# Performance work log

Measured on AMD Instinct MI355X. Metric: run time of the kernel, lower is better.

The kernel has to match this reference:

```python
import jax, jax.numpy as jnp
import numpy as np

B, S, D_IN = 2, 2048, 1024
H = 16
HD = 64  # head_dim = d_out // head_cnt


def setup_inputs() -> dict:
    key = jax.random.key(0)
    kx, kq, kk, kv = jax.random.split(key, 4)
    x = jax.random.normal(kx, (B, S, D_IN), dtype=jnp.float32)
    # Per-head Q/K/V projection weights, stacked: [H, d_in, head_dim].
    # Matches nn.Linear(d_in, head_out) per head (qkv_bias=False), scaled like
    # a typical init.
    sc = 1.0 / np.sqrt(D_IN)
    Wq = jax.random.normal(kq, (H, D_IN, HD), dtype=jnp.float32) * sc
    Wk = jax.random.normal(kk, (H, D_IN, HD), dtype=jnp.float32) * sc
    Wv = jax.random.normal(kv, (H, D_IN, HD), dtype=jnp.float32) * sc
    return {"x": x, "Wq": Wq, "Wk": Wk, "Wv": Wv}


def reference(x, Wq, Wk, Wv):
    # Batched multi-head causal attention equivalent to the per-head loop +
    # torch.cat(dim=-1): head h's output occupies slice [h*HD:(h+1)*HD].
    q = jnp.einsum("bsd,hde->bhse", x, Wq)  # [B,H,S,HD]
    k = jnp.einsum("bsd,hde->bhse", x, Wk)
    v = jnp.einsum("bsd,hde->bhse", x, Wv)
    scale = 1.0 / jnp.sqrt(jnp.asarray(HD, dtype=x.dtype))
    scores = jnp.einsum("bhse,bhte->bhst", q, k) * scale  # [B,H,S,S]
    seq = x.shape[1]
    causal = jnp.tril(jnp.ones((seq, seq), dtype=bool))
    scores = jnp.where(causal, scores, jnp.asarray(-jnp.inf, dtype=scores.dtype))
    attn = jax.nn.softmax(scores, axis=-1)  # dropout = 0.0 -> identity
    ctx = jnp.einsum("bhst,bhte->bhse", attn, v)  # [B,H,S,HD]
    # concat heads on last dim
    b, h, s, e = ctx.shape
    return ctx.transpose(0, 2, 1, 3).reshape(b, s, h * e)
```

## Files before the change

kernel.cpp:

```cpp
#include <hip/hip_runtime.h>


#define DI   1024
#define HD   64
#define NH   16
#define SEQ  2048
#define NB   2

typedef unsigned short u16;
typedef unsigned short us8 __attribute__((ext_vector_type(8)));
typedef unsigned short us4 __attribute__((ext_vector_type(4)));
typedef unsigned int   u32x2 __attribute__((ext_vector_type(2)));
typedef short bf8 __attribute__((ext_vector_type(8)));
typedef float f4 __attribute__((ext_vector_type(4)));
typedef float f16v __attribute__((ext_vector_type(16)));

#define MFMA16(a, b, c) __builtin_amdgcn_mfma_f32_16x16x32_bf16((a), (b), (c), 0, 0, 0)
#define MFMA32(a, b, c) __builtin_amdgcn_mfma_f32_32x32x16_bf16((a), (b), (c), 0, 0, 0)

#if __has_builtin(__builtin_amdgcn_exp2f)
#define EXP2(x) __builtin_amdgcn_exp2f(x)
#else
#define EXP2(x) exp2f(x)
#endif

#if __has_builtin(__builtin_amdgcn_perm)
#define PKHI(a, b) __builtin_amdgcn_perm((a), (b), 0x07060302u)
#else
__device__ __forceinline__ unsigned PKHI(unsigned a, unsigned b) {
  return (b >> 16) | (a & 0xffff0000u);
}
#endif

__device__ __forceinline__ u16 f2bf(float f) {
  unsigned u = __float_as_uint(f);
  u += 0x7fffu + ((u >> 16) & 1u);
  return (u16)(u >> 16);
}

__device__ __forceinline__ void async16(const u16* g, u16* l) {
  __builtin_amdgcn_global_load_lds((const __attribute__((address_space(1))) void*)g,
                                   (__attribute__((address_space(3))) void*)l,
                                   16, 0, 0);
}

__global__ __launch_bounds__(256) void prep_k(const float* __restrict__ x,
                                              const float* __restrict__ Wq,
                                              const float* __restrict__ Wk,
                                              const float* __restrict__ Wv,
                                              u16* __restrict__ xb,
                                              u16* __restrict__ Wt) {
  __shared__ __align__(16) u16 tile[64][72];
  const int bid = blockIdx.x;
  if (bid < 2048) {
    const int i = (bid * 256 + threadIdx.x) * 8;
    float4 v0 = *(const float4*)(x + i);
    float4 v1 = *(const float4*)(x + i + 4);
    us8 o;
    o[0] = f2bf(v0.x); o[1] = f2bf(v0.y); o[2] = f2bf(v0.z); o[3] = f2bf(v0.w);
    o[4] = f2bf(v1.x); o[5] = f2bf(v1.y); o[6] = f2bf(v1.z); o[7] = f2bf(v1.w);
    *(us8*)(xb + i) = o;
    return;
  }
  const int idx = bid - 2048;
  const int mh = idx >> 4;
  const int d0 = (idx & 15) * 64;
  const int mat = mh >> 4, h = mh & 15;
  const float* W = (mat == 0 ? Wq : (mat == 1 ? Wk : Wv)) + (size_t)h * DI * HD;
  const int t = threadIdx.x;
  {
    const int r = t >> 2, c = (t & 3) * 16;
    const float* src = W + (size_t)(d0 + r) * HD + c;
    #pragma unroll
    for (int j = 0; j < 4; j++) {
      float4 v = *(const float4*)(src + j * 4);
      tile[r][c + j * 4 + 0] = f2bf(v.x);
      tile[r][c + j * 4 + 1] = f2bf(v.y);
      tile[r][c + j * 4 + 2] = f2bf(v.z);
      tile[r][c + j * 4 + 3] = f2bf(v.w);
    }
  }
  __syncthreads();
  {
    const int e = t >> 2, c = (t & 3) * 16;
    __align__(16) u16 tmp[16];
    #pragma unroll
    for (int i = 0; i < 16; i++) tmp[i] = tile[c + i][e];
    u16* dst = Wt + ((size_t)mh * HD + e) * DI + d0 + c;
    *(us8*)dst       = *(us8*)&tmp[0];
    *(us8*)(dst + 8) = *(us8*)&tmp[8];
  }
}

__global__ __launch_bounds__(256, 2) void proj_k(const u16* __restrict__ x,
                                                 const u16* __restrict__ Wt,
                                                 u16* __restrict__ Qo,
                                                 u16* __restrict__ Ko,
                                                 u16* __restrict__ Vo) {
  __shared__ __align__(16) u16 smem[40960];
  u16* const xs = smem;
  u16* const ws = smem + 16384;
  const int m0 = blockIdx.x * 128, n0 = blockIdx.y * 192;
  const int tid = threadIdx.x, w = tid >> 6, lane = tid & 63;
  const int l15 = lane & 15, quad = lane >> 4, l7 = l15 & 7;
  const int lrow = lane >> 3, lch = lane & 7;
  const int wm = w >> 1, wn = w & 1;

  f4 acc[4][6];
  #pragma unroll
  for (int i = 0; i < 4; i++)
    #pragma unroll
    for (int j = 0; j < 6; j++) {
      f4 z = {0.f, 0.f, 0.f, 0.f};
      acc[i][j] = z;
    }

  const u16* xg = x  + (size_t)(m0 + lrow) * DI + ((lch ^ lrow) * 8);
  const u16* wg = Wt + (size_t)(n0 + lrow) * DI + ((lch ^ lrow) * 8);

  #pragma unroll
  for (int i = 0; i < 4; i++)
    async16(xg + (size_t)(i * 32 + w * 8) * DI, &xs[(i * 32 + w * 8) * 64]);
  #pragma unroll
  for (int c = 0; c < 6; c++)
    async16(wg + (size_t)(w * 48 + c * 8) * DI, &ws[(w * 48 + c * 8) * 64]);

  for (int it = 0; it < 16; it++) {
    const int cbx = (it & 1) * 8192, cbw = (it & 1) * 12288;
    __syncthreads();
    if (it + 1 < 16) {
      const int k1 = (it + 1) * 64;
      const int nbx = 8192 - cbx, nbw = 12288 - cbw;
      #pragma unroll
      for (int i = 0; i < 4; i++)
        async16(xg + (size_t)(i * 32 + w * 8) * DI + k1,
                &xs[nbx + (i * 32 + w * 8) * 64]);
      #pragma unroll
      for (int c = 0; c < 6; c++)
        async16(wg + (size_t)(w * 48 + c * 8) * DI + k1,
                &ws[nbw + (w * 48 + c * 8) * 64]);
    }
    #pragma unroll
    for (int ks = 0; ks < 64; ks += 32) {
      const int c0 = (ks >> 3) + quad;
      bf8 af[4], bfr[6];
      #pragma unroll
      for (int i = 0; i < 4; i++)
        af[i] = *(const bf8*)&xs[cbx + (wm * 64 + i * 16 + l15) * 64 + ((c0 ^ l7) * 8)];
      #pragma unroll
      for (int i = 0; i < 6; i++)
        bfr[i] = *(const bf8*)&ws[cbw + (wn * 96 + i * 16 + l15) * 64 + ((c0 ^ l7) * 8)];
      #pragma unroll
      for (int mi = 0; mi < 4; mi++)
        #pragma unroll
        for (int ni = 0; ni < 6; ni++)
          acc[mi][ni] = MFMA16(af[mi], bfr[ni], acc[mi][ni]);
    }
  }

  const float qscale = 0.125f * 1.44269504088896340736f;
  #pragma unroll
  for (int mi = 0; mi < 4; mi++) {
    const int mrow = m0 + wm * 64 + mi * 16 + quad * 4;
    const int b = mrow >> 11, sb = mrow & (SEQ - 1);
    #pragma unroll
    for (int ni = 0; ni < 6; ni++) {
      const int nf = n0 + wn * 96 + ni * 16;
      const int mat = nf >> 10;
      const int h = (nf >> 6) & 15;
      const int e = (nf & 63) + l15;
      if (mat == 2) {
        __align__(8) u16 pk[4];
        #pragma unroll
        for (int r = 0; r < 4; r++) pk[r] = f2bf(acc[mi][ni][r]);
        *(us4*)(Vo + (((size_t)b * NH + h) * HD + e) * SEQ + sb) = *(us4*)pk;
      } else {
        u16* O = mat ? Ko : Qo;
        const float sc = mat ? 1.0f : qscale;
        #pragma unroll
        for (int r = 0; r < 4; r++)
          O[(((size_t)b * NH + h) * SEQ + sb + r) * HD + e] = f2bf(acc[mi][ni][r] * sc);
      }
    }
  }
}

__global__ __launch_bounds__(256, 2) void attn_k(const u16* __restrict__ Qo,
                                                 const u16* __restrict__ Ko,
                                                 const u16* __restrict__ Vo,
                                                 float* __restrict__ out) {
  __shared__ __align__(16) u16 Ks[2 * 128 * 64];
  __shared__ __align__(16) u16 Vs[2 * 64 * 128];
  __shared__ float Ls[128];
  const int bh = blockIdx.x;
  const int y  = blockIdx.y;
  const int t  = (y < 8) ? y : 23 - y;
  const int b = bh >> 4, h = bh & 15;
  const int tid = threadIdx.x, w = tid >> 6, lane = tid & 63;
  const int l31 = lane & 31, hi = lane >> 5;
  const int k7 = l31 & 7, v15 = l31 & 15;
  const int nI = t + 1;

  const u16* Qb = Qo + (size_t)bh * SEQ * HD;
  const u16* Kb = Ko + (size_t)bh * SEQ * HD;
  const u16* Vb = Vo + (size_t)bh * HD * SEQ;

  const int kl = lane >> 3, kc = lane & 7;
  const int vl = lane >> 4, vc = lane & 15;
  const int mq = w * 32 + l31;

  bf8 bq[4];
  #pragma unroll
  for (int ks = 0; ks < 4; ks++)
    bq[ks] = *(const bf8*)(Qb + (size_t)(t * 128 + w * 32 + l31) * HD + ks * 16 + hi * 8);

  f16v o0, o1, zf;
  #pragma unroll
  for (int i = 0; i < 16; i++) { o0[i] = 0.f; o1[i] = 0.f; zf[i] = 0.f; }
  float lsum = 0.f;

  const u16* kg = Kb + (size_t)(w * 32 + kl) * HD + ((kc ^ kl) * 8);
  const u16* vg[4];
  u16* ldsK[4];
  u16* ldsV[4];
  #pragma unroll
  for (int i = 0; i < 4; i++) {
    const int vr = w * 16 + i * 4;
    const int f = (i * 4 + vl) & 15;
    vg[i] = Vb + (size_t)(vr + vl) * SEQ + ((vc ^ f) * 8);
    ldsK[i] = &Ks[(w * 32 + i * 8) * 64];
    ldsV[i] = &Vs[vr * 128];
  }

  #pragma unroll
  for (int i = 0; i < 4; i++) {
    async16(kg + i * 512, ldsK[i]);
    async16(vg[i], ldsV[i]);
  }
  kg += 128 * HD;
  #pragma unroll
  for (int i = 0; i < 4; i++) vg[i] += 128;

  for (int it = 0; it < nI; ++it) {
    const int cb = (it & 1) * 8192;
    __syncthreads();
    if (it + 1 < nI) {
      const int nb = 8192 - cb;
      #pragma unroll
      for (int i = 0; i < 4; i++) {
        async16(kg + i * 512, ldsK[i] + nb);
        async16(vg[i], ldsV[i] + nb);
      }
      kg += 128 * HD;
      #pragma unroll
      for (int i = 0; i < 4; i++) vg[i] += 128;
    }
    const bool domask = (it == nI - 1);

    #pragma unroll
    for (int mf = 0; mf < 4; mf++) {
      f16v s;
      __builtin_amdgcn_s_setprio(1);
      {
        bf8 ak = *(const bf8*)&Ks[cb + mf * 2048 + l31 * 64 + ((hi ^ k7) * 8)];
        s = MFMA32(ak, bq[0], zf);
      }
      #pragma unroll
      for (int ks = 1; ks < 4; ks++) {
        bf8 ak = *(const bf8*)&Ks[cb + mf * 2048 + l31 * 64 + (((2 * ks + hi) ^ k7) * 8)];
        s = MFMA32(ak, bq[ks], s);
      }
      __builtin_amdgcn_s_setprio(0);

      unsigned pu[16];
      #pragma unroll
      for (int r = 0; r < 16; r++) {
        float pv = EXP2(s[r]);
        if (domask) {
          const int kt = mf * 32 + (r & 3) + 8 * (r >> 2) + 4 * hi;
          pv = (kt <= mq) ? pv : 0.f;
        }
        lsum += pv;
        pu[r] = __float_as_uint(pv);
      }
      unsigned a0 = PKHI(pu[1],  pu[0]),  a1 = PKHI(pu[3],  pu[2]);
      unsigned a2 = PKHI(pu[5],  pu[4]),  a3 = PKHI(pu[7],  pu[6]);
      unsigned a4 = PKHI(pu[9],  pu[8]),  a5 = PKHI(pu[11], pu[10]);
      unsigned a6 = PKHI(pu[13], pu[12]), a7 = PKHI(pu[15], pu[14]);
      asm("v_permlane32_swap_b32 %0, %1" : "+v"(a0), "+v"(a2));
      asm("v_permlane32_swap_b32 %0, %1" : "+v"(a1), "+v"(a3));
      asm("v_permlane32_swap_b32 %0, %1" : "+v"(a4), "+v"(a6));
      asm("v_permlane32_swap_b32 %0, %1" : "+v"(a5), "+v"(a7));
      bf8 pf0, pf1;
      ((unsigned*)&pf0)[0] = a0; ((unsigned*)&pf0)[1] = a1;
      ((unsigned*)&pf0)[2] = a2; ((unsigned*)&pf0)[3] = a3;
      ((unsigned*)&pf1)[0] = a4; ((unsigned*)&pf1)[1] = a5;
      ((unsigned*)&pf1)[2] = a6; ((unsigned*)&pf1)[3] = a7;

      __builtin_amdgcn_s_setprio(1);
      {
        const int c0 = ((4 * mf + hi) ^ v15) * 8;
        bf8 vf0 = *(const bf8*)&Vs[cb + l31 * 128 + c0];
        bf8 vf1 = *(const bf8*)&Vs[cb + 4096 + l31 * 128 + c0];
        o0 = MFMA32(pf0, vf0, o0);
        o1 = MFMA32(pf0, vf1, o1);
      }
      {
        const int c1 = ((4 * mf + 2 + hi) ^ v15) * 8;
        bf8 vf0 = *(const bf8*)&Vs[cb + l31 * 128 + c1];
        bf8 vf1 = *(const bf8*)&Vs[cb + 4096 + l31 * 128 + c1];
        o0 = MFMA32(pf1, vf0, o0);
        o1 = MFMA32(pf1, vf1, o1);
      }
      __builtin_amdgcn_s_setprio(0);
    }
  }

  const float lt = lsum + __shfl_xor(lsum, 32, 64);
  if (hi == 0) Ls[w * 32 + l31] = lt;
  __syncthreads();

  float* op = out + ((size_t)(b * SEQ + t * 128 + w * 32)) * (NH * HD) + h * HD + l31;
  #pragma unroll
  for (int r = 0; r < 16; r++) {
    const int qr = (r & 3) + 8 * (r >> 2) + 4 * hi;
    const float linv = 1.0f / Ls[w * 32 + qr];
    op[(size_t)qr * (NH * HD)]      = o0[r] * linv;
    op[(size_t)qr * (NH * HD) + 32] = o1[r] * linv;
  }
}

extern "C" void kernel_launch(void* const* d_in, const int* in_sizes, int n_in,
                              void* d_out, int out_size, void* d_ws, size_t ws_size,
                              hipStream_t stream) {
  const float* x  = (const float*)d_in[0];
  const float* Wq = (const float*)d_in[1];
  const float* Wk = (const float*)d_in[2];
  const float* Wv = (const float*)d_in[3];
  float* out = (float*)d_out;

  u16* xb = (u16*)d_ws;
  u16* Wt = xb + (size_t)NB * SEQ * DI;
  u16* Qo = Wt + (size_t)3 * NH * HD * DI;
  u16* Ko = Qo + (size_t)NB * NH * SEQ * HD;
  u16* Vo = Ko + (size_t)NB * NH * SEQ * HD;

  prep_k<<<dim3(2048 + 768), 256, 0, stream>>>(x, Wq, Wk, Wv, xb, Wt);
  proj_k<<<dim3(32, 16), 256, 0, stream>>>(xb, Wt, Qo, Ko, Vo);
  attn_k<<<dim3(32, 16), 256, 0, stream>>>(Qo, Ko, Vo, out);
}
```

Measured before the change: 139.2 us.

## Shrink projection GEMM tile to 128x128 with BK32 and repacked LDS swizzle

The QKV projection kernel now uses 128x128 output tiles with a 32-wide K step instead of 128x192 with a 64-wide K step. Shared memory drops from 80 KB to 32 KB, and the launch bound asks for 3 blocks per CU. The grid grows from 512 to 768 blocks. The LDS layout is also repacked so that two 32-element tile rows share one 64-element row, using a new XOR swizzle for loads and fragment reads. The aim is to fill the GPU better and raise occupancy, at the cost of less operand reuse per tile and twice as many K iterations and barriers.

```diff
diff --git a/kernel.cpp b/kernel.cpp
--- a/kernel.cpp
+++ b/kernel.cpp
@@ -92,70 +92,70 @@
   }
 }
 
-__global__ __launch_bounds__(256, 2) void proj_k(const u16* __restrict__ x,
+__global__ __launch_bounds__(256, 3) void proj_k(const u16* __restrict__ x,
                                                  const u16* __restrict__ Wt,
                                                  u16* __restrict__ Qo,
                                                  u16* __restrict__ Ko,
                                                  u16* __restrict__ Vo) {
-  __shared__ __align__(16) u16 smem[40960];
+  __shared__ __align__(16) u16 smem[16384];
   u16* const xs = smem;
-  u16* const ws = smem + 16384;
-  const int m0 = blockIdx.x * 128, n0 = blockIdx.y * 192;
+  u16* const ws = smem + 8192;
+  const int m0 = blockIdx.x * 128, n0 = blockIdx.y * 128;
   const int tid = threadIdx.x, w = tid >> 6, lane = tid & 63;
-  const int l15 = lane & 15, quad = lane >> 4, l7 = l15 & 7;
-  const int lrow = lane >> 3, lch = lane & 7;
+  const int l15 = lane & 15, quad = lane >> 4;
   const int wm = w >> 1, wn = w & 1;
 
-  f4 acc[4][6];
+  f4 acc[4][4];
   #pragma unroll
   for (int i = 0; i < 4; i++)
     #pragma unroll
-    for (int j = 0; j < 6; j++) {
+    for (int j = 0; j < 4; j++) {
       f4 z = {0.f, 0.f, 0.f, 0.f};
       acc[i][j] = z;
     }
 
-  const u16* xg = x  + (size_t)(m0 + lrow) * DI + ((lch ^ lrow) * 8);
-  const u16* wg = Wt + (size_t)(n0 + lrow) * DI + ((lch ^ lrow) * 8);
-
-  #pragma unroll
-  for (int i = 0; i < 4; i++)
-    async16(xg + (size_t)(i * 32 + w * 8) * DI, &xs[(i * 32 + w * 8) * 64]);
-  #pragma unroll
-  for (int c = 0; c < 6; c++)
-    async16(wg + (size_t)(w * 48 + c * 8) * DI, &ws[(w * 48 + c * 8) * 64]);
-
-  for (int it = 0; it < 16; it++) {
-    const int cbx = (it & 1) * 8192, cbw = (it & 1) * 12288;
+  const int sr8 = lane >> 3, c7 = lane & 7;
+  const int g8 = c7 ^ (sr8 & 7);
+  const int row16 = sr8 * 2 + (g8 >> 2);
+  const int kc = g8 & 3;
+
+  const u16* xg = x  + (size_t)(m0 + w * 16 + row16) * DI + kc * 8;
+  const u16* wg = Wt + (size_t)(n0 + w * 16 + row16) * DI + kc * 8;
+
+  const int rsw = ((((l15 & 1) << 2) + quad) ^ (l15 >> 1)) * 8;
+  const int rA = wm * 32 + (l15 >> 1);
+  const int rB = wn * 32 + (l15 >> 1);
+
+  #pragma unroll
+  for (int i = 0; i < 2; i++) {
+    async16(xg + (size_t)(i * 64) * DI, &xs[(i * 64 + w * 16) * 32]);
+    async16(wg + (size_t)(i * 64) * DI, &ws[(i * 64 + w * 16) * 32]);
+  }
+
+  for (int it = 0; it < 32; it++) {
+    const int cb = (it & 1) * 4096;
     __syncthreads();
-    if (it + 1 < 16) {
-      const int k1 = (it + 1) * 64;
-      const int nbx = 8192 - cbx, nbw = 12288 - cbw;
-      #pragma unroll
-      for (int i = 0; i < 4; i++)
-        async16(xg + (size_t)(i * 32 + w * 8) * DI + k1,
-                &xs[nbx + (i * 32 + w * 8) * 64]);
-      #pragma unroll
-      for (int c = 0; c < 6; c++)
-        async16(wg + (size_t)(w * 48 + c * 8) * DI + k1,
-                &ws[nbw + (w * 48 + c * 8) * 64]);
-    }
-    #pragma unroll
-    for (int ks = 0; ks < 64; ks += 32) {
-      const int c0 = (ks >> 3) + quad;
-      bf8 af[4], bfr[6];
-      #pragma unroll
-      for (int i = 0; i < 4; i++)
-        af[i] = *(const bf8*)&xs[cbx + (wm * 64 + i * 16 + l15) * 64 + ((c0 ^ l7) * 8)];
-      #pragma unroll
-      for (int i = 0; i < 6; i++)
-        bfr[i] = *(const bf8*)&ws[cbw + (wn * 96 + i * 16 + l15) * 64 + ((c0 ^ l7) * 8)];
-      #pragma unroll
-      for (int mi = 0; mi < 4; mi++)
-        #pragma unroll
-        for (int ni = 0; ni < 6; ni++)
-          acc[mi][ni] = MFMA16(af[mi], bfr[ni], acc[mi][ni]);
-    }
+    if (it + 1 < 32) {
+      const int k1 = (it + 1) * 32;
+      const int nb = 4096 - cb;
+      #pragma unroll
+      for (int i = 0; i < 2; i++) {
+        async16(xg + (size_t)(i * 64) * DI + k1, &xs[nb + (i * 64 + w * 16) * 32]);
+        async16(wg + (size_t)(i * 64) * DI + k1, &ws[nb + (i * 64 + w * 16) * 32]);
+      }
+    }
+    bf8 af[4], bfr[4];
+    #pragma unroll
+    for (int i = 0; i < 4; i++)
+      af[i] = *(const bf8*)&xs[cb + (rA + i * 8) * 64 + rsw];
+    #pragma unroll
+    for (int i = 0; i < 4; i++)
+      bfr[i] = *(const bf8*)&ws[cb + (rB + i * 8) * 64 + rsw];
+    #pragma unroll
+    for (int mi = 0; mi < 4; mi++)
+      #pragma unroll
+      for (int ni = 0; ni < 4; ni++)
+        acc[mi][ni] = MFMA16(af[mi], bfr[ni], acc[mi][ni]);
   }
 
   const float qscale = 0.125f * 1.44269504088896340736f;
@@ -164,8 +164,8 @@
     const int mrow = m0 + wm * 64 + mi * 16 + quad * 4;
     const int b = mrow >> 11, sb = mrow & (SEQ - 1);
     #pragma unroll
-    for (int ni = 0; ni < 6; ni++) {
-      const int nf = n0 + wn * 96 + ni * 16;
+    for (int ni = 0; ni < 4; ni++) {
+      const int nf = n0 + wn * 64 + ni * 16;
       const int mat = nf >> 10;
       const int h = (nf >> 6) & 15;
       const int e = (nf & 63) + l15;
@@ -346,6 +346,6 @@
   u16* Vo = Ko + (size_t)NB * NH * SEQ * HD;
 
   prep_k<<<dim3(2048 + 768), 256, 0, stream>>>(x, Wq, Wk, Wv, xb, Wt);
-  proj_k<<<dim3(32, 16), 256, 0, stream>>>(xb, Wt, Qo, Ko, Vo);
+  proj_k<<<dim3(32, 24), 256, 0, stream>>>(xb, Wt, Qo, Ko, Vo);
   attn_k<<<dim3(32, 16), 256, 0, stream>>>(Qo, Ko, Vo, out);
 }
```

Measured after the change: 144.1 us. 1.03x slower.

## Load K/V fragments directly from global memory instead of staging through LDS

Applied to the files above, without the earlier changes.

Removes the double-buffered LDS staging of K and V tiles, the async copies and the per-iteration __syncthreads. Each wave now reads its MFMA operand fragments for K and V straight from global memory, relying on L1/L2 caching. This drops the LDS traffic and block-level synchronisation and relaxes the launch bound. In exchange, all four waves read the same K/V data from global memory separately, and without explicit prefetching the load latency sits directly in front of the MFMAs.

```diff
diff --git a/kernel.cpp b/kernel.cpp
--- a/kernel.cpp
+++ b/kernel.cpp
@@ -185,12 +185,10 @@
   }
 }
 
-__global__ __launch_bounds__(256, 2) void attn_k(const u16* __restrict__ Qo,
-                                                 const u16* __restrict__ Ko,
-                                                 const u16* __restrict__ Vo,
-                                                 float* __restrict__ out) {
-  __shared__ __align__(16) u16 Ks[2 * 128 * 64];
-  __shared__ __align__(16) u16 Vs[2 * 64 * 128];
+__global__ __launch_bounds__(256) void attn_k(const u16* __restrict__ Qo,
+                                              const u16* __restrict__ Ko,
+                                              const u16* __restrict__ Vo,
+                                              float* __restrict__ out) {
   __shared__ float Ls[128];
   const int bh = blockIdx.x;
   const int y  = blockIdx.y;
@@ -198,15 +196,12 @@
   const int b = bh >> 4, h = bh & 15;
   const int tid = threadIdx.x, w = tid >> 6, lane = tid & 63;
   const int l31 = lane & 31, hi = lane >> 5;
-  const int k7 = l31 & 7, v15 = l31 & 15;
   const int nI = t + 1;
 
   const u16* Qb = Qo + (size_t)bh * SEQ * HD;
   const u16* Kb = Ko + (size_t)bh * SEQ * HD;
   const u16* Vb = Vo + (size_t)bh * HD * SEQ;
 
-  const int kl = lane >> 3, kc = lane & 7;
-  const int vl = lane >> 4, vc = lane & 15;
   const int mq = w * 32 + l31;
 
   bf8 bq[4];
@@ -219,55 +214,27 @@
   for (int i = 0; i < 16; i++) { o0[i] = 0.f; o1[i] = 0.f; zf[i] = 0.f; }
   float lsum = 0.f;
 
-  const u16* kg = Kb + (size_t)(w * 32 + kl) * HD + ((kc ^ kl) * 8);
-  const u16* vg[4];
-  u16* ldsK[4];
-  u16* ldsV[4];
-  #pragma unroll
-  for (int i = 0; i < 4; i++) {
-    const int vr = w * 16 + i * 4;
-    const int f = (i * 4 + vl) & 15;
-    vg[i] = Vb + (size_t)(vr + vl) * SEQ + ((vc ^ f) * 8);
-    ldsK[i] = &Ks[(w * 32 + i * 8) * 64];
-    ldsV[i] = &Vs[vr * 128];
-  }
-
-  #pragma unroll
-  for (int i = 0; i < 4; i++) {
-    async16(kg + i * 512, ldsK[i]);
-    async16(vg[i], ldsV[i]);
-  }
-  kg += 128 * HD;
-  #pragma unroll
-  for (int i = 0; i < 4; i++) vg[i] += 128;
+  const u16* kf   = Kb + (size_t)l31 * HD + hi * 8;
+  const u16* vf0p = Vb + (size_t)l31 * SEQ + hi * 8;
+  const u16* vf1p = vf0p + (size_t)32 * SEQ;
 
   for (int it = 0; it < nI; ++it) {
-    const int cb = (it & 1) * 8192;
-    __syncthreads();
-    if (it + 1 < nI) {
-      const int nb = 8192 - cb;
-      #pragma unroll
-      for (int i = 0; i < 4; i++) {
-        async16(kg + i * 512, ldsK[i] + nb);
-        async16(vg[i], ldsV[i] + nb);
-      }
-      kg += 128 * HD;
-      #pragma unroll
-      for (int i = 0; i < 4; i++) vg[i] += 128;
-    }
     const bool domask = (it == nI - 1);
+    const u16* kit  = kf   + (size_t)it * 128 * HD;
+    const u16* v0it = vf0p + it * 128;
+    const u16* v1it = vf1p + it * 128;
 
     #pragma unroll
     for (int mf = 0; mf < 4; mf++) {
       f16v s;
       __builtin_amdgcn_s_setprio(1);
       {
-        bf8 ak = *(const bf8*)&Ks[cb + mf * 2048 + l31 * 64 + ((hi ^ k7) * 8)];
+        bf8 ak = *(const bf8*)(kit + mf * 32 * HD);
         s = MFMA32(ak, bq[0], zf);
       }
       #pragma unroll
       for (int ks = 1; ks < 4; ks++) {
-        bf8 ak = *(const bf8*)&Ks[cb + mf * 2048 + l31 * 64 + (((2 * ks + hi) ^ k7) * 8)];
+        bf8 ak = *(const bf8*)(kit + mf * 32 * HD + ks * 16);
         s = MFMA32(ak, bq[ks], s);
       }
       __builtin_amdgcn_s_setprio(0);
@@ -299,18 +266,16 @@
 
       __builtin_amdgcn_s_setprio(1);
       {
-        const int c0 = ((4 * mf + hi) ^ v15) * 8;
-        bf8 vf0 = *(const bf8*)&Vs[cb + l31 * 128 + c0];
-        bf8 vf1 = *(const bf8*)&Vs[cb + 4096 + l31 * 128 + c0];
-        o0 = MFMA32(pf0, vf0, o0);
-        o1 = MFMA32(pf0, vf1, o1);
+        bf8 va = *(const bf8*)(v0it + mf * 32);
+        bf8 vb = *(const bf8*)(v1it + mf * 32);
+        o0 = MFMA32(pf0, va, o0);
+        o1 = MFMA32(pf0, vb, o1);
       }
       {
-        const int c1 = ((4 * mf + 2 + hi) ^ v15) * 8;
-        bf8 vf0 = *(const bf8*)&Vs[cb + l31 * 128 + c1];
-        bf8 vf1 = *(const bf8*)&Vs[cb + 4096 + l31 * 128 + c1];
-        o0 = MFMA32(pf1, vf0, o0);
-        o1 = MFMA32(pf1, vf1, o1);
+        bf8 va = *(const bf8*)(v0it + mf * 32 + 16);
+        bf8 vb = *(const bf8*)(v1it + mf * 32 + 16);
+        o0 = MFMA32(pf1, va, o0);
+        o1 = MFMA32(pf1, vb, o1);
       }
       __builtin_amdgcn_s_setprio(0);
     }
```

Result: slower. 180.2 us (+29.4%).

## Compute softmax row sums via MFMA with ones and split accumulators

Applied to the files above, without the earlier changes.

Replaces the scalar per-lane row-sum accumulation and the LDS/shuffle reduction with extra MFMA ops that multiply the bf16 probabilities by a ones vector, so the denominator lands in the same layout as the output. Output accumulators are split into two independent chains to break MFMA dependency, and the occupancy hint of 2 is dropped from launch bounds. The cost is 50% more MFMA work and many more accumulator registers (seven 16-float vectors), which can lower occupancy. The denominator now sums bf16-rounded probabilities, which matches the numerator's precision.

```diff
diff --git a/kernel.cpp b/kernel.cpp
--- a/kernel.cpp
+++ b/kernel.cpp
@@ -185,13 +185,12 @@
   }
 }
 
-__global__ __launch_bounds__(256, 2) void attn_k(const u16* __restrict__ Qo,
-                                                 const u16* __restrict__ Ko,
-                                                 const u16* __restrict__ Vo,
-                                                 float* __restrict__ out) {
+__global__ __launch_bounds__(256) void attn_k(const u16* __restrict__ Qo,
+                                              const u16* __restrict__ Ko,
+                                              const u16* __restrict__ Vo,
+                                              float* __restrict__ out) {
   __shared__ __align__(16) u16 Ks[2 * 128 * 64];
   __shared__ __align__(16) u16 Vs[2 * 64 * 128];
-  __shared__ float Ls[128];
   const int bh = blockIdx.x;
   const int y  = blockIdx.y;
   const int t  = (y < 8) ? y : 23 - y;
@@ -214,10 +213,14 @@
   for (int ks = 0; ks < 4; ks++)
     bq[ks] = *(const bf8*)(Qb + (size_t)(t * 128 + w * 32 + l31) * HD + ks * 16 + hi * 8);
 
-  f16v o0, o1, zf;
-  #pragma unroll
-  for (int i = 0; i < 16; i++) { o0[i] = 0.f; o1[i] = 0.f; zf[i] = 0.f; }
-  float lsum = 0.f;
+  f16v o0a, o0b, o1a, o1b, la0, la1, zf;
+  #pragma unroll
+  for (int i = 0; i < 16; i++) {
+    o0a[i] = 0.f; o0b[i] = 0.f; o1a[i] = 0.f; o1b[i] = 0.f;
+    la0[i] = 0.f; la1[i] = 0.f; zf[i] = 0.f;
+  }
+  const bf8 ones = {0x3F80, 0x3F80, 0x3F80, 0x3F80,
+                    0x3F80, 0x3F80, 0x3F80, 0x3F80};
 
   const u16* kg = Kb + (size_t)(w * 32 + kl) * HD + ((kc ^ kl) * 8);
   const u16* vg[4];
@@ -280,7 +283,6 @@
           const int kt = mf * 32 + (r & 3) + 8 * (r >> 2) + 4 * hi;
           pv = (kt <= mq) ? pv : 0.f;
         }
-        lsum += pv;
         pu[r] = __float_as_uint(pv);
       }
       unsigned a0 = PKHI(pu[1],  pu[0]),  a1 = PKHI(pu[3],  pu[2]);
@@ -302,31 +304,29 @@
         const int c0 = ((4 * mf + hi) ^ v15) * 8;
         bf8 vf0 = *(const bf8*)&Vs[cb + l31 * 128 + c0];
         bf8 vf1 = *(const bf8*)&Vs[cb + 4096 + l31 * 128 + c0];
-        o0 = MFMA32(pf0, vf0, o0);
-        o1 = MFMA32(pf0, vf1, o1);
+        o0a = MFMA32(pf0, vf0, o0a);
+        o1a = MFMA32(pf0, vf1, o1a);
+        la0 = MFMA32(pf0, ones, la0);
       }
       {
         const int c1 = ((4 * mf + 2 + hi) ^ v15) * 8;
         bf8 vf0 = *(const bf8*)&Vs[cb + l31 * 128 + c1];
         bf8 vf1 = *(const bf8*)&Vs[cb + 4096 + l31 * 128 + c1];
-        o0 = MFMA32(pf1, vf0, o0);
-        o1 = MFMA32(pf1, vf1, o1);
+        o0b = MFMA32(pf1, vf0, o0b);
+        o1b = MFMA32(pf1, vf1, o1b);
+        la1 = MFMA32(pf1, ones, la1);
       }
       __builtin_amdgcn_s_setprio(0);
     }
   }
-
-  const float lt = lsum + __shfl_xor(lsum, 32, 64);
-  if (hi == 0) Ls[w * 32 + l31] = lt;
-  __syncthreads();
 
   float* op = out + ((size_t)(b * SEQ + t * 128 + w * 32)) * (NH * HD) + h * HD + l31;
   #pragma unroll
   for (int r = 0; r < 16; r++) {
     const int qr = (r & 3) + 8 * (r >> 2) + 4 * hi;
-    const float linv = 1.0f / Ls[w * 32 + qr];
-    op[(size_t)qr * (NH * HD)]      = o0[r] * linv;
-    op[(size_t)qr * (NH * HD) + 32] = o1[r] * linv;
+    const float linv = 1.0f / (la0[r] + la1[r]);
+    op[(size_t)qr * (NH * HD)]      = (o0a[r] + o0b[r]) * linv;
+    op[(size_t)qr * (NH * HD) + 32] = (o1a[r] + o1b[r]) * linv;
   }
 }
 
```

Result: slower. 143.0 us (+2.7%).
